# Performance work log

Measured on AMD Instinct MI355X. Metric: run time of the kernel, lower is better.

Reference implementation:

```python
import jax, jax.numpy as jnp
import numpy as np

B, N, D_IN, D_OUT, R = 8, 1024, 256, 256, 4


def setup_inputs() -> dict:
    key = jax.random.key(0)
    ks = jax.random.split(key, 8)
    scale_in = 1.0 / np.sqrt(D_IN)
    scale_out = 1.0 / np.sqrt(2 * D_OUT)
    scale_g = 1.0 / np.sqrt(D_OUT)
    return {
        "node_features": jax.random.normal(ks[0], (B, N, D_IN), dtype=jnp.float32),
        "adj_matrix": jax.random.randint(ks[1], (B, R, N, N), 0, 2, dtype=jnp.int32),
        "rel_w": jax.random.uniform(ks[2], (R, D_OUT, D_IN), jnp.float32, -scale_in, scale_in),
        "rel_b": jax.random.uniform(ks[3], (R, D_OUT), jnp.float32, -scale_in, scale_in),
        "attn_w": jax.random.uniform(ks[4], (2 * D_OUT,), jnp.float32, -scale_out, scale_out),
        "attn_b": jax.random.uniform(ks[5], (), jnp.float32, -scale_out, scale_out),
        "gate_w": jax.random.uniform(ks[6], (D_OUT,), jnp.float32, -scale_g, scale_g),
        "gate_b": jax.random.uniform(ks[7], (), jnp.float32, -scale_g, scale_g),
    }


def reference(node_features, adj_matrix, rel_w, rel_b, attn_w, attn_b, gate_w, gate_b):
    # Per-relation projections: [B, R, N, D]
    feats = jnp.einsum('bni,rdi->brnd', node_features, rel_w) + rel_b[None, :, None, :]
    # attn_proj(cat([h_i, h_j])) == h_i @ w_i + h_j @ w_j + b  (linear over concat)
    d = feats.shape[-1]
    si = jnp.einsum('brnd,d->brn', feats, attn_w[:d])   # contribution of row node i
    sj = jnp.einsum('brnd,d->brn', feats, attn_w[d:])   # contribution of col node j
    score = si[:, :, :, None] + sj[:, :, None, :] + attn_b  # [B, R, N, N]
    score = jnp.where(adj_matrix == 0, jnp.float32(-1e9), score)
    attn = jax.nn.softmax(score, axis=-1)
    # Aggregate over relations: sum_r attn_r @ feats_r -> [B, N, D]
    agg = jnp.einsum('brnm,brmd->bnd', attn, feats)
    gate = jax.nn.sigmoid(jnp.einsum('bnd,d->bn', agg, gate_w) + gate_b)
    return gate[:, :, None] * agg
```

## Files before the change

### kernel.cpp

```cpp
#include <hip/hip_runtime.h>
#include <hip/hip_bf16.h>

#define B_ 8
#define N_ 1024
#define DIN 256
#define DOUT 256
#define R_ 4

typedef __attribute__((ext_vector_type(8))) short bf16x8;
typedef __attribute__((ext_vector_type(4))) float f32x4;
typedef __attribute__((ext_vector_type(4))) int i32x4;

__device__ __forceinline__ unsigned short f2bf(float f) {
    union { float f; unsigned int u; } v; v.f = f;
    unsigned int u = v.u;
    u += 0x7fffu + ((u >> 16) & 1u);
    return (unsigned short)(u >> 16);
}
__device__ __forceinline__ float bf2f(unsigned short h) {
    union { float f; unsigned int u; } v; v.u = ((unsigned int)h) << 16;
    return v.f;
}

__device__ __forceinline__ void gl_lds16(const void* g, void* l) {
    __builtin_amdgcn_global_load_lds(
        (const __attribute__((address_space(1))) unsigned int*)g,
        (__attribute__((address_space(3))) unsigned int*)l, 16, 0, 0);
}

__global__ __launch_bounds__(256) void k0_swz(const float* __restrict__ rw,
                                              unsigned short* __restrict__ swzW) {
    int t = blockIdx.x * 256 + threadIdx.x;
    int lane = t & 63, nb = (t >> 6) & 15, ks = (t >> 10) & 7, r = t >> 13;
    int m = lane & 15, q = lane >> 4;
    const float* src = rw + ((r * DOUT + nb * 16 + m) * DIN) + ks * 32 + q * 8;
    float4 v0 = *(const float4*)src;
    float4 v1 = *(const float4*)(src + 4);
    bf16x8 o;
    o[0] = (short)f2bf(v0.x); o[1] = (short)f2bf(v0.y);
    o[2] = (short)f2bf(v0.z); o[3] = (short)f2bf(v0.w);
    o[4] = (short)f2bf(v1.x); o[5] = (short)f2bf(v1.y);
    o[6] = (short)f2bf(v1.z); o[7] = (short)f2bf(v1.w);
    *(bf16x8*)(swzW + (long)t * 8) = o;
}

__global__ __launch_bounds__(256) void k1_proj(const float* __restrict__ node,
        const unsigned short* __restrict__ swzW, const float* __restrict__ rel_b,
        const float* __restrict__ attn_w,
        unsigned short* __restrict__ fswz, unsigned short* __restrict__ ebf) {
    __shared__ unsigned short Wbuf[2][8192];
    int bid = blockIdx.x;
    int nt = bid & 15, r = (bid >> 4) & 3, b = bid >> 6;
    int w = threadIdx.x >> 6, lane = threadIdx.x & 63;
    int m = lane & 15, q = lane >> 4;
    int n0 = nt * 64 + w * 16;

    const float* Abase = node + ((b * N_ + n0 + m) * DIN) + q * 8;
    const unsigned short* Wsrc = swzW + r * 65536;

#pragma unroll
    for (int i = 0; i < 4; i++)
        gl_lds16(Wsrc + (w * 4 + i) * 512 + lane * 8, &Wbuf[0][(w * 4 + i) * 512]);

    f32x4 acc[16];
#pragma unroll
    for (int i = 0; i < 16; i++) acc[i] = (f32x4)0.0f;

    float4 a0 = *(const float4*)(Abase);
    float4 a1 = *(const float4*)(Abase + 4);

    for (int ks = 0; ks < 8; ks++) {
        int cur = ks & 1;
        __syncthreads();
        if (ks < 7) {
#pragma unroll
            for (int i = 0; i < 4; i++)
                gl_lds16(Wsrc + ((ks + 1) * 16 + w * 4 + i) * 512 + lane * 8,
                         &Wbuf[cur ^ 1][(w * 4 + i) * 512]);
        }
        bf16x8 af;
        af[0] = (short)f2bf(a0.x); af[1] = (short)f2bf(a0.y);
        af[2] = (short)f2bf(a0.z); af[3] = (short)f2bf(a0.w);
        af[4] = (short)f2bf(a1.x); af[5] = (short)f2bf(a1.y);
        af[6] = (short)f2bf(a1.z); af[7] = (short)f2bf(a1.w);
        if (ks < 7) {
            a0 = *(const float4*)(Abase + (ks + 1) * 32);
            a1 = *(const float4*)(Abase + (ks + 1) * 32 + 4);
        }
#pragma unroll
        for (int nb = 0; nb < 16; nb++) {
            bf16x8 wf = *(const bf16x8*)(&Wbuf[cur][nb * 512 + lane * 8]);
            acc[nb] = __builtin_amdgcn_mfma_f32_16x16x32_bf16(af, wf, acc[nb], 0, 0, 0);
        }
    }

    float sj0 = 0.f, sj1 = 0.f, sj2 = 0.f, sj3 = 0.f;
    float bias[16], aw[16];
#pragma unroll
    for (int nb = 0; nb < 16; nb++) {
        int d = nb * 16 + m;
        bias[nb] = rel_b[r * DOUT + d];
        aw[nb] = attn_w[DOUT + d];
        sj0 += (acc[nb][0] + bias[nb]) * aw[nb];
        sj1 += (acc[nb][1] + bias[nb]) * aw[nb];
        sj2 += (acc[nb][2] + bias[nb]) * aw[nb];
        sj3 += (acc[nb][3] + bias[nb]) * aw[nb];
    }
#pragma unroll
    for (int mk = 1; mk <= 8; mk <<= 1) {
        sj0 += __shfl_xor(sj0, mk, 64);
        sj1 += __shfl_xor(sj1, mk, 64);
        sj2 += __shfl_xor(sj2, mk, 64);
        sj3 += __shfl_xor(sj3, mk, 64);
    }
    float e0 = __expf(sj0), e1 = __expf(sj1), e2 = __expf(sj2), e3 = __expf(sj3);

    int slice = b * R_ + r;
    int js = n0 >> 5;
    int jhi = (n0 >> 4) & 1;
    int qp = jhi * 2 + (q >> 1);
    int jj0 = (q & 1) * 4;
    unsigned short* fb = fswz + ((long)(slice * 32 + js) * 16) * 512
                       + qp * 128 + m * 8 + jj0;
#pragma unroll
    for (int nb = 0; nb < 16; nb++) {
        ushort4 o;
        o.x = f2bf((acc[nb][0] + bias[nb]) * e0);
        o.y = f2bf((acc[nb][1] + bias[nb]) * e1);
        o.z = f2bf((acc[nb][2] + bias[nb]) * e2);
        o.w = f2bf((acc[nb][3] + bias[nb]) * e3);
        *(ushort4*)(fb + nb * 512) = o;
    }
    if (m == 0) {
        ushort4 o;
        o.x = f2bf(e0); o.y = f2bf(e1); o.z = f2bf(e2); o.w = f2bf(e3);
        *(ushort4*)(ebf + slice * N_ + n0 + q * 4) = o;
    }
}

__global__ __launch_bounds__(256) void k2_pack(const int* __restrict__ adj,
                                               unsigned int* __restrict__ pk) {
    int t = blockIdx.x * 256 + threadIdx.x;
    const int* src = adj + (size_t)t * 32;
    i32x4 v[8];
#pragma unroll
    for (int i = 0; i < 8; i++) v[i] = *(const i32x4*)(src + i * 4);
    unsigned int bits = 0;
#pragma unroll
    for (int i = 0; i < 8; i++) {
        bits |= (v[i].x ? 1u : 0u) << (4 * i);
        bits |= (v[i].y ? 2u : 0u) << (4 * i);
        bits |= (v[i].z ? 4u : 0u) << (4 * i);
        bits |= (v[i].w ? 8u : 0u) << (4 * i);
    }
    pk[t] = bits;
}

__global__ __launch_bounds__(256, 4) void k3_attn(const unsigned int* __restrict__ pk,
        const unsigned short* __restrict__ fswz, const unsigned short* __restrict__ ebf,
        unsigned short* __restrict__ aggU, float* __restrict__ lbuf) {
    __shared__ unsigned short Gbuf[2][8192];
    __shared__ unsigned short Ebuf[512];

    int bid = blockIdx.x;
    int slice = (bid & 7) * 4 + ((bid >> 3) & 3);
    int rest = bid >> 5;
    int it = rest & 15, jh = rest >> 4;
    int t = threadIdx.x, lane = t & 63, w = t >> 6;
    int m = lane & 15, q = lane >> 4;
    int i0b = it * 64;

    const unsigned short* fsl = fswz + ((size_t)(slice * 32 + jh * 16)) * 8192;
    const unsigned short* esl = ebf + slice * N_ + jh * 512;

    const unsigned int* pb = pk + ((size_t)slice * N_ + i0b + w * 16 + m) * 32 + jh * 16;
    unsigned int Wv[16];
    *(i32x4*)(&Wv[0])  = *(const i32x4*)(pb);
    *(i32x4*)(&Wv[4])  = *(const i32x4*)(pb + 4);
    *(i32x4*)(&Wv[8])  = *(const i32x4*)(pb + 8);
    *(i32x4*)(&Wv[12]) = *(const i32x4*)(pb + 12);
    int q8 = q * 8;

#pragma unroll
    for (int i = 0; i < 4; i++)
        gl_lds16(fsl + (w * 4 + i) * 512 + lane * 8, &Gbuf[0][(w * 4 + i) * 512]);
    if (w == 0)
        gl_lds16(esl + lane * 8, &Ebuf[0]);

    f32x4 acc[16];
#pragma unroll
    for (int i = 0; i < 16; i++) acc[i] = (f32x4)0.0f;
    float l = 0.f;

#pragma unroll
    for (int s = 0; s < 16; s++) {
        int cur = s & 1;
        __syncthreads();
        if (s < 15) {
#pragma unroll
            for (int i = 0; i < 4; i++)
                gl_lds16(fsl + (size_t)(s + 1) * 8192 + (w * 4 + i) * 512 + lane * 8,
                         &Gbuf[cur ^ 1][(w * 4 + i) * 512]);
        }
        unsigned int byte = (Wv[s] >> q8) & 0xffu;
        bf16x8 ev = *(const bf16x8*)(&Ebuf[s * 32 + q * 8]);
        const int* ei = (const int*)&ev;
        bf16x8 af;
        int* afi = (int*)&af;
#pragma unroll
        for (int p = 0; p < 4; p++) {
            unsigned int msk = (((byte >> (2 * p)) & 1u) ? 0xffffu : 0u)
                             | (((byte >> (2 * p + 1)) & 1u) ? 0xffff0000u : 0u);
            afi[p] = (int)(msk & 0x3F803F80u);
            int me = ei[p] & (int)msk;
            union { int i; float f; } lo, hi;
            lo.i = me << 16;
            hi.i = me & (int)0xffff0000u;
            l += lo.f + hi.f;
        }
        const unsigned short* Gb = &Gbuf[cur][lane * 8];
#pragma unroll
        for (int nb = 0; nb < 16; nb++) {
            bf16x8 bfq = *(const bf16x8*)(Gb + nb * 512);
            acc[nb] = __builtin_amdgcn_mfma_f32_16x16x32_bf16(af, bfq, acc[nb], 0, 0, 0);
        }
    }

    l += __shfl_xor(l, 16, 64);
    l += __shfl_xor(l, 32, 64);
    int half = slice * 2 + jh;
    if (lane < 16)
        lbuf[half * N_ + i0b + w * 16 + lane] = l;

    unsigned short* ob = aggU + ((size_t)half * N_ + i0b + w * 16 + q * 4) * DOUT + m;
#pragma unroll
    for (int nb = 0; nb < 16; nb++) {
#pragma unroll
        for (int reg = 0; reg < 4; reg++)
            ob[(size_t)reg * DOUT + nb * 16] = f2bf(acc[nb][reg]);
    }
}

__global__ __launch_bounds__(256) void k4_out(const unsigned short* __restrict__ aggU,
        const float* __restrict__ lbuf, const float* __restrict__ gate_w,
        const float* __restrict__ gate_b, float* __restrict__ out) {
    __shared__ float red[4];
    int bid = blockIdx.x;
    int n = bid & 1023, b = bid >> 10;
    int d = threadIdx.x;
    float s = 0.f;
#pragma unroll
    for (int r = 0; r < R_; r++) {
        int sl = b * R_ + r;
        float a0 = bf2f(aggU[((size_t)(sl * 2 + 0) * N_ + n) * DOUT + d]);
        float a1 = bf2f(aggU[((size_t)(sl * 2 + 1) * N_ + n) * DOUT + d]);
        float lt = lbuf[(sl * 2 + 0) * N_ + n] + lbuf[(sl * 2 + 1) * N_ + n];
        float inv = (lt > 0.f) ? 1.0f / lt : 0.f;
        s += (a0 + a1) * inv;
    }
    float v = s * gate_w[d];
#pragma unroll
    for (int off = 32; off; off >>= 1) v += __shfl_down(v, off, 64);
    int lane = d & 63, wave = d >> 6;
    if (lane == 0) red[wave] = v;
    __syncthreads();
    float tot = red[0] + red[1] + red[2] + red[3];
    float g = 1.f / (1.f + __expf(-(tot + gate_b[0])));
    out[((long)(b * N_ + n)) * DOUT + d] = g * s;
}

extern "C" void kernel_launch(void* const* d_in, const int* in_sizes, int n_in,
                              void* d_out, int out_size, void* d_ws, size_t ws_size,
                              hipStream_t stream) {
    const float* node   = (const float*)d_in[0];
    const int*   adj    = (const int*)d_in[1];
    const float* rel_w  = (const float*)d_in[2];
    const float* rel_b  = (const float*)d_in[3];
    const float* attn_w = (const float*)d_in[4];
    const float* gate_w = (const float*)d_in[6];
    const float* gate_b = (const float*)d_in[7];
    float* out = (float*)d_out;

    char* ws = (char*)d_ws;
    unsigned short* swzW = (unsigned short*)ws;
    unsigned short* fswz = (unsigned short*)(ws + 524288);
    unsigned short* ebf  = (unsigned short*)(ws + 17301504);
    unsigned short* aggU = (unsigned short*)(ws + 17367040);
    float*          lbuf = (float*)(ws + 50921472);
    unsigned int*   pk   = (unsigned int*)(ws + 51183616);

    k0_swz<<<128, 256, 0, stream>>>(rel_w, swzW);
    k2_pack<<<4096, 256, 0, stream>>>(adj, pk);
    k1_proj<<<512, 256, 0, stream>>>(node, swzW, rel_b, attn_w, fswz, ebf);
    k3_attn<<<1024, 256, 0, stream>>>(pk, fswz, ebf, aggU, lbuf);
    k4_out<<<8192, 256, 0, stream>>>(aggU, lbuf, gate_w, gate_b, out);
}
```

Baseline: 276.9 us.

## Process two 64-row tiles per block in attention kernel to reuse feature tiles

Each k3_attn block now computes 128 query rows (two 64-row sub-tiles) instead of 64, so every shared-memory feature tile is used by twice as many MFMAs and global feature loads are halved. The grid shrinks from 1024 to 512 blocks and launch bounds drop from 4 to 2 waves per SIMD to allow the doubled accumulator registers. The cost is fewer resident blocks and less latency hiding, with lower occupancy on a 256-CU device.

```diff
diff --git a/kernel.cpp b/kernel.cpp
--- a/kernel.cpp
+++ b/kernel.cpp
@@ -156,7 +156,7 @@
     pk[t] = bits;
 }
 
-__global__ __launch_bounds__(256, 4) void k3_attn(const unsigned int* __restrict__ pk,
+__global__ __launch_bounds__(256, 2) void k3_attn(const unsigned int* __restrict__ pk,
         const unsigned short* __restrict__ fswz, const unsigned short* __restrict__ ebf,
         unsigned short* __restrict__ aggU, float* __restrict__ lbuf) {
     __shared__ unsigned short Gbuf[2][8192];
@@ -165,20 +165,21 @@
     int bid = blockIdx.x;
     int slice = (bid & 7) * 4 + ((bid >> 3) & 3);
     int rest = bid >> 5;
-    int it = rest & 15, jh = rest >> 4;
+    int pair = rest & 7, jh = rest >> 3;
     int t = threadIdx.x, lane = t & 63, w = t >> 6;
     int m = lane & 15, q = lane >> 4;
-    int i0b = it * 64;
+    int i0b = pair * 128;
 
     const unsigned short* fsl = fswz + ((size_t)(slice * 32 + jh * 16)) * 8192;
     const unsigned short* esl = ebf + slice * N_ + jh * 512;
 
-    const unsigned int* pb = pk + ((size_t)slice * N_ + i0b + w * 16 + m) * 32 + jh * 16;
-    unsigned int Wv[16];
-    *(i32x4*)(&Wv[0])  = *(const i32x4*)(pb);
-    *(i32x4*)(&Wv[4])  = *(const i32x4*)(pb + 4);
-    *(i32x4*)(&Wv[8])  = *(const i32x4*)(pb + 8);
-    *(i32x4*)(&Wv[12]) = *(const i32x4*)(pb + 12);
+    const unsigned int* pA = pk + ((size_t)slice * N_ + i0b + w * 16 + m) * 32 + jh * 16;
+    const unsigned int* pB = pA + 64 * 32;
+    unsigned int Wa[16], Wb[16];
+#pragma unroll
+    for (int i = 0; i < 4; i++) *(i32x4*)(&Wa[i * 4]) = *(const i32x4*)(pA + i * 4);
+#pragma unroll
+    for (int i = 0; i < 4; i++) *(i32x4*)(&Wb[i * 4]) = *(const i32x4*)(pB + i * 4);
     int q8 = q * 8;
 
 #pragma unroll
@@ -187,10 +188,10 @@
     if (w == 0)
         gl_lds16(esl + lane * 8, &Ebuf[0]);
 
-    f32x4 acc[16];
-#pragma unroll
-    for (int i = 0; i < 16; i++) acc[i] = (f32x4)0.0f;
-    float l = 0.f;
+    f32x4 accA[16], accB[16];
+#pragma unroll
+    for (int i = 0; i < 16; i++) { accA[i] = (f32x4)0.0f; accB[i] = (f32x4)0.0f; }
+    float lA = 0.f, lB = 0.f;
 
 #pragma unroll
     for (int s = 0; s < 16; s++) {
@@ -202,42 +203,57 @@
                 gl_lds16(fsl + (size_t)(s + 1) * 8192 + (w * 4 + i) * 512 + lane * 8,
                          &Gbuf[cur ^ 1][(w * 4 + i) * 512]);
         }
-        unsigned int byte = (Wv[s] >> q8) & 0xffu;
+        unsigned int byteA = (Wa[s] >> q8) & 0xffu;
+        unsigned int byteB = (Wb[s] >> q8) & 0xffu;
         bf16x8 ev = *(const bf16x8*)(&Ebuf[s * 32 + q * 8]);
         const int* ei = (const int*)&ev;
-        bf16x8 af;
-        int* afi = (int*)&af;
+        bf16x8 afA, afB;
+        int* aiA = (int*)&afA;
+        int* aiB = (int*)&afB;
 #pragma unroll
         for (int p = 0; p < 4; p++) {
-            unsigned int msk = (((byte >> (2 * p)) & 1u) ? 0xffffu : 0u)
-                             | (((byte >> (2 * p + 1)) & 1u) ? 0xffff0000u : 0u);
-            afi[p] = (int)(msk & 0x3F803F80u);
-            int me = ei[p] & (int)msk;
+            unsigned int mA = (((byteA >> (2 * p)) & 1u) ? 0xffffu : 0u)
+                            | (((byteA >> (2 * p + 1)) & 1u) ? 0xffff0000u : 0u);
+            unsigned int mB = (((byteB >> (2 * p)) & 1u) ? 0xffffu : 0u)
+                            | (((byteB >> (2 * p + 1)) & 1u) ? 0xffff0000u : 0u);
+            aiA[p] = (int)(mA & 0x3F803F80u);
+            aiB[p] = (int)(mB & 0x3F803F80u);
+            int meA = ei[p] & (int)mA;
+            int meB = ei[p] & (int)mB;
             union { int i; float f; } lo, hi;
-            lo.i = me << 16;
-            hi.i = me & (int)0xffff0000u;
-            l += lo.f + hi.f;
+            lo.i = meA << 16; hi.i = meA & (int)0xffff0000u;
+            lA += lo.f + hi.f;
+            lo.i = meB << 16; hi.i = meB & (int)0xffff0000u;
+            lB += lo.f + hi.f;
         }
         const unsigned short* Gb = &Gbuf[cur][lane * 8];
 #pragma unroll
         for (int nb = 0; nb < 16; nb++) {
             bf16x8 bfq = *(const bf16x8*)(Gb + nb * 512);
-            acc[nb] = __builtin_amdgcn_mfma_f32_16x16x32_bf16(af, bfq, acc[nb], 0, 0, 0);
-        }
-    }
-
-    l += __shfl_xor(l, 16, 64);
-    l += __shfl_xor(l, 32, 64);
+            accA[nb] = __builtin_amdgcn_mfma_f32_16x16x32_bf16(afA, bfq, accA[nb], 0, 0, 0);
+            accB[nb] = __builtin_amdgcn_mfma_f32_16x16x32_bf16(afB, bfq, accB[nb], 0, 0, 0);
+        }
+    }
+
+    lA += __shfl_xor(lA, 16, 64);
+    lA += __shfl_xor(lA, 32, 64);
+    lB += __shfl_xor(lB, 16, 64);
+    lB += __shfl_xor(lB, 32, 64);
     int half = slice * 2 + jh;
-    if (lane < 16)
-        lbuf[half * N_ + i0b + w * 16 + lane] = l;
-
-    unsigned short* ob = aggU + ((size_t)half * N_ + i0b + w * 16 + q * 4) * DOUT + m;
+    if (lane < 16) {
+        lbuf[half * N_ + i0b + w * 16 + lane] = lA;
+        lbuf[half * N_ + i0b + 64 + w * 16 + lane] = lB;
+    }
+
+    unsigned short* obA = aggU + ((size_t)half * N_ + i0b + w * 16 + q * 4) * DOUT + m;
+    unsigned short* obB = obA + (size_t)64 * DOUT;
 #pragma unroll
     for (int nb = 0; nb < 16; nb++) {
 #pragma unroll
-        for (int reg = 0; reg < 4; reg++)
-            ob[(size_t)reg * DOUT + nb * 16] = f2bf(acc[nb][reg]);
+        for (int reg = 0; reg < 4; reg++) {
+            obA[(size_t)reg * DOUT + nb * 16] = f2bf(accA[nb][reg]);
+            obB[(size_t)reg * DOUT + nb * 16] = f2bf(accB[nb][reg]);
+        }
     }
 }
 
@@ -292,6 +308,6 @@
     k0_swz<<<128, 256, 0, stream>>>(rel_w, swzW);
     k2_pack<<<4096, 256, 0, stream>>>(adj, pk);
     k1_proj<<<512, 256, 0, stream>>>(node, swzW, rel_b, attn_w, fswz, ebf);
-    k3_attn<<<1024, 256, 0, stream>>>(pk, fswz, ebf, aggU, lbuf);
+    k3_attn<<<512, 256, 0, stream>>>(pk, fswz, ebf, aggU, lbuf);
     k4_out<<<8192, 256, 0, stream>>>(aggU, lbuf, gate_w, gate_b, out);
 }
```

Measured after the change: 256.8 us. 7.3% less time.
